# Performance work log

Hardware: AMD Instinct MI355X
Metric: run time of the kernel (lower is better)

## Reference

```python
import jax, jax.numpy as jnp
import numpy as np


def setup_inputs() -> dict:
    key = jax.random.key(0)
    k1, k2, k3, k4 = jax.random.split(key, 4)
    b, h, t, dim, topk = 16, 8, 196, 512, 49
    x = jax.random.normal(k1, (b, t, dim), dtype=jnp.float32)
    adj = jax.random.normal(k2, (b, h, t, t), dtype=jnp.float32)  # per-head routing logits
    Wqkv = jax.random.normal(k3, (dim, 3 * dim), dtype=jnp.float32) * 0.02
    Wv = jax.random.normal(k4, (dim, dim), dtype=jnp.float32) * 0.02
    return {"x": x, "adj": adj, "Wqkv": Wqkv, "Wv": Wv, "topk": topk}


def reference(x, adj, Wqkv, Wv, topk):
    b, t, dim = x.shape
    h = adj.shape[1]
    d = dim // h
    scale = dim ** (-0.5)  # note: full dim, matching source (self.scale = dim**-0.5)

    # qkv projection (stand-in for GIN conv_proj_qkv with nhid = 3*dim)
    qkv = (x @ Wqkv).reshape(b, t, h, 3 * d).transpose(0, 2, 1, 3)  # b h t 3d
    q, k, v = jnp.split(qkv, 3, axis=-1)  # each b h t d

    # TopkRouting: indices of top-k routing logits per (b, h, query-token)
    _, r_idx = jax.lax.top_k(adj, topk)  # b h t topk (r_weight unused: mul_weight='none')

    # KGather: irregular gather of concatenated k/v rows per query token
    kv = jnp.concatenate([k, v], axis=-1).reshape(b * h, t, 2 * d)
    idx = r_idx.reshape(b * h, t, topk)
    kv_sel = jax.vmap(lambda m, i: m[i])(kv, idx)          # (bh, t, topk, 2d)
    kv_sel = kv_sel.reshape(b, h, t, topk, 2 * d)
    k_sel, v_sel = jnp.split(kv_sel, 2, axis=-1)            # b h t topk d

    # small-window attention: each query attends to its topk gathered rows (w^2 = 1)
    attn = jax.nn.softmax(jnp.einsum('bhtd,bhtkd->bhtk', q * scale, k_sel), axis=-1)
    o = jnp.einsum('bhtk,bhtkd->bhtd', attn, v_sel)

    o = o.transpose(0, 2, 1, 3).reshape(b, t, dim)
    o = jax.nn.gelu(o, approximate=False)  # torch F.gelu default = exact erf
    return o @ Wv
```

## Files before the change

### kernel.cpp

```cpp
#include <hip/hip_runtime.h>
#include <hip/hip_bf16.h>
#include <cmath>

#define B_   16
#define H_   8
#define T_   196
#define DIM_ 512
#define DHEAD_ 64
#define TOPK_ 49
#define BT_  (B_ * T_)
#define BH_  (B_ * H_)

#define QB_OFF   0u
#define KB_OFF   1605632u
#define VT_OFF   3211264u
#define XB_OFF   5046272u
#define WQKVT_OFF 6651904u
#define WVT_OFF  7438336u
#define MASK_OFF 7700480u

typedef __bf16 bf16x8 __attribute__((ext_vector_type(8)));
typedef float f32x4 __attribute__((ext_vector_type(4)));

__device__ __forceinline__ unsigned short f2bf(float f) {
    union { float f; unsigned int u; } v; v.f = f;
    const unsigned int u = v.u;
    return (unsigned short)((u + 0x7FFFu + ((u >> 16) & 1u)) >> 16);
}

__device__ __forceinline__ unsigned int ordered_u32(float f) {
    int i = __float_as_int(f);
    return (i < 0) ? ~(unsigned int)i : ((unsigned int)i | 0x80000000u);
}

__device__ __forceinline__ void gload16(const void* g, void* l) {
    __builtin_amdgcn_global_load_lds(
        (const __attribute__((address_space(1))) unsigned int*)g,
        (__attribute__((address_space(3))) unsigned int*)l, 16, 0, 0);
}

__device__ __forceinline__ void route_topk_q(const float* __restrict__ adj,
                                             unsigned int* __restrict__ masks,
                                             const int q, const int lane) {
    const float* arow = adj + (size_t)q * T_;
    const bool v3 = (lane < 4);
    unsigned int u[4];
    u[0] = ordered_u32(arow[lane]);
    u[1] = ordered_u32(arow[lane + 64]);
    u[2] = ordered_u32(arow[lane + 128]);
    u[3] = v3 ? ordered_u32(arow[lane + 192]) : 0u;

    unsigned int w0 = u[0], w1 = u[1], w2 = u[2], w3 = u[3];
    unsigned int prefix = 0u, thr = 0u;
    int k = TOPK_, A = T_;
    for (int b = 31; b >= 0; --b) {
        int C1 = 0;
        C1 += __popcll(__ballot((w0 >> b) == 1u));
        C1 += __popcll(__ballot((w1 >> b) == 1u));
        C1 += __popcll(__ballot((w2 >> b) == 1u));
        C1 += __popcll(__ballot((w3 >> b) == 1u));
        if (C1 >= k) {
            const unsigned int bit = 1u << b;
            prefix |= bit;
            w0 ^= bit; w1 ^= bit; w2 ^= bit; w3 ^= bit;
            A = C1;
        } else { k -= C1; A -= C1; }

        if (k == A || k == 1) {
            const bool mx = (k == 1);
            unsigned int best = mx ? 0u : 0xFFFFFFFFu;
            const unsigned int ww[4] = {w0, w1, w2, w3};
#pragma unroll
            for (int s2 = 0; s2 < 4; ++s2) {
                const bool valid = (s2 < 3) || v3;
                const bool act = valid && ((ww[s2] >> b) == 0u);
                if (act) best = mx ? (u[s2] > best ? u[s2] : best)
                                   : (u[s2] < best ? u[s2] : best);
            }
#pragma unroll
            for (int off = 32; off >= 1; off >>= 1) {
                const unsigned int o = __shfl_xor(best, off);
                best = mx ? (o > best ? o : best) : (o < best ? o : best);
            }
            thr = best;
            break;
        }
        if (b == 0) thr = prefix;
    }

    const unsigned long long lmask = (1ull << lane) - 1ull;
    unsigned long long gm[4];
    int G = 0;
#pragma unroll
    for (int s2 = 0; s2 < 4; ++s2) {
        const bool valid = (s2 < 3) || v3;
        gm[s2] = __ballot(valid && (u[s2] > thr));
        G += __popcll(gm[s2]);
    }
    const int need = TOPK_ - G;
    int cum = 0;
    unsigned long long sb0 = 0, sb1 = 0, sb2 = 0, sb3 = 0;
#pragma unroll
    for (int s2 = 0; s2 < 4; ++s2) {
        const bool valid = (s2 < 3) || v3;
        const bool e = valid && (u[s2] == thr);
        const unsigned long long em = __ballot(e);
        const int rk = cum + __popcll(em & lmask);
        cum += __popcll(em);
        const unsigned long long sel = gm[s2] | __ballot(e && (rk < need));
        if (s2 == 0) sb0 = sel; else if (s2 == 1) sb1 = sel;
        else if (s2 == 2) sb2 = sel; else sb3 = sel;
    }
    if (lane < 8) {
        const unsigned long long mv = (lane < 2) ? sb0 : (lane < 4) ? sb1
                                    : (lane < 6) ? sb2 : sb3;
        const unsigned int wd = (lane & 1) ? (unsigned int)(mv >> 32) : (unsigned int)mv;
        masks[(size_t)q * 8 + lane] = wd;
    }
}

__global__ __launch_bounds__(256) void prep(const float* __restrict__ x,
                                            const float* __restrict__ Wqkv,
                                            unsigned short* __restrict__ xb,
                                            unsigned short* __restrict__ wqkvT) {
    __shared__ unsigned short Tt[64][72];
    const int t = threadIdx.x;
    const int bid = blockIdx.x;

    if (bid < 784) {
        const size_t base = ((size_t)bid * 256 + t) * 8;
        const float4 v0 = *(const float4*)&x[base];
        const float4 v1 = *(const float4*)&x[base + 4];
        uint4 pk;
        pk.x = (unsigned int)f2bf(v0.x) | ((unsigned int)f2bf(v0.y) << 16);
        pk.y = (unsigned int)f2bf(v0.z) | ((unsigned int)f2bf(v0.w) << 16);
        pk.z = (unsigned int)f2bf(v1.x) | ((unsigned int)f2bf(v1.y) << 16);
        pk.w = (unsigned int)f2bf(v1.z) | ((unsigned int)f2bf(v1.w) << 16);
        *(uint4*)&xb[base] = pk;
        return;
    }

    const int b = bid - 784;
    const int tx = b % 24, ty = b / 24;
    const int c0 = tx * 64, r0 = ty * 64;
#pragma unroll
    for (int p = 0; p < 4; ++p) {
        const int r = (t >> 4) + 16 * p;
        const int cl = (t & 15) * 4;
        const float4 v = *(const float4*)&Wqkv[(size_t)(r0 + r) * 1536 + c0 + cl];
        Tt[cl + 0][r] = f2bf(v.x);
        Tt[cl + 1][r] = f2bf(v.y);
        Tt[cl + 2][r] = f2bf(v.z);
        Tt[cl + 3][r] = f2bf(v.w);
    }
    __syncthreads();
#pragma unroll
    for (int p = 0; p < 2; ++p) {
        const int cc = (t >> 3) + 32 * p;
        const int ch = (t & 7) * 8;
        *(uint4*)&wqkvT[(size_t)(c0 + cc) * 512 + r0 + ch] = *(const uint4*)&Tt[cc][ch];
    }
}

template <int BN, int MODE, int FUSE, typename CT>
__global__ __launch_bounds__(256) void gemm_mfma(const unsigned short* __restrict__ A,
                                                 const unsigned short* __restrict__ Bt,
                                                 CT* __restrict__ C,
                                                 const int M, const int N, const int K,
                                                 const float* __restrict__ adj,
                                                 unsigned int* __restrict__ masks,
                                                 unsigned short* __restrict__ vT,
                                                 const float* __restrict__ Wv,
                                                 unsigned short* __restrict__ wvT) {
    constexpr int FN = BN / 32;
    constexpr int CSZ = (MODE == 1) ? 64 * 132 : 1;
    struct ABt { unsigned short A[64][32]; unsigned short B[BN][32]; };
    __shared__ union {
        ABt ab[2];
        unsigned short Cs[CSZ];
        unsigned short Tt[FUSE ? 64 : 1][72];
    } sm;

    const int tid = threadIdx.x;
    const int lane = tid & 63, wid = tid >> 6;
    const int mt = M >> 6;
    const int nGemm = mt * (N / BN);
    const int bid = blockIdx.x;

    if constexpr (FUSE) {
        if (bid >= nGemm) {
            const int rid = bid - nGemm;
            if (rid < 6272) {
                route_topk_q(adj, masks, rid * 4 + wid, lane);
            } else if (rid < 6300) {
                const int e0 = (rid - 6272) * 8192 + tid;
#pragma unroll
                for (int i = 0; i < 32; ++i) {
                    const int e = e0 + i * 256;
                    const int bh = e / 1792;
                    const int rem = e - bh * 1792;
                    const int d = rem / 28;
                    const int tt = rem - d * 28;
                    vT[(size_t)bh * (64 * 224) + (size_t)d * 224 + 196 + tt] = 0;
                }
            } else {
                const int b = rid - 6300;
                const int tx = b & 7, ty = b >> 3;
                const int c0 = tx * 64, r0 = ty * 64;
#pragma unroll
                for (int p = 0; p < 4; ++p) {
                    const int r = (tid >> 4) + 16 * p;
                    const int cl = (tid & 15) * 4;
                    const float4 v = *(const float4*)&Wv[(size_t)(r0 + r) * 512 + c0 + cl];
                    sm.Tt[cl + 0][r] = f2bf(v.x);
                    sm.Tt[cl + 1][r] = f2bf(v.y);
                    sm.Tt[cl + 2][r] = f2bf(v.z);
                    sm.Tt[cl + 3][r] = f2bf(v.w);
                }
                __syncthreads();
#pragma unroll
                for (int p = 0; p < 2; ++p) {
                    const int cc = (tid >> 3) + 32 * p;
                    const int ch = (tid & 7) * 8;
                    *(uint4*)&wvT[(size_t)(c0 + cc) * 512 + r0 + ch] =
                        *(const uint4*)&sm.Tt[cc][ch];
                }
            }
            return;
        }
    }

    const int bx = bid % mt;
    const int by = bid / mt;
    const int row0 = bx * 64;
    const int col0 = by * BN;
    const int wr = wid >> 1, wc = wid & 1;

    f32x4 acc[2][FN];
#pragma unroll
    for (int m = 0; m < 2; ++m)
#pragma unroll
        for (int n = 0; n < FN; ++n)
            acc[m][n] = (f32x4){0.0f, 0.0f, 0.0f, 0.0f};

    const int srow = lane >> 2;
    const int scol = (lane & 3) * 8;
    const unsigned short* aSrc = A + (size_t)(row0 + wid * 16 + srow) * K + scol;
    const unsigned short* bSrc = Bt + (size_t)(col0 + wid * 16 + srow) * K + scol;
    const unsigned short* bSrc2 = bSrc + (size_t)64 * K;

    const int fr = lane & 15;
    const int fk8 = (lane >> 4) * 8;

#define STAGE(BUF) do {                                                        \
        gload16(aSrc, &sm.ab[BUF].A[wid * 16][0]);                             \
        gload16(bSrc, &sm.ab[BUF].B[wid * 16][0]);                             \
        if constexpr (BN == 128) gload16(bSrc2, &sm.ab[BUF].B[64 + wid * 16][0]); \
        aSrc += 32; bSrc += 32; bSrc2 += 32;                                   \
    } while (0)

#define COMPUTE(BUF) do {                                                      \
        bf16x8 af[2], bfv[FN];                                                 \
        _Pragma("unroll")                                                      \
        for (int m = 0; m < 2; ++m)                                            \
            af[m] = *(const bf16x8*)&sm.ab[BUF].A[wr * 32 + m * 16 + fr][fk8]; \
        _Pragma("unroll")                                                      \
        for (int n = 0; n < FN; ++n)                                           \
            bfv[n] = *(const bf16x8*)&sm.ab[BUF].B[wc * (BN / 2) + n * 16 + fr][fk8]; \
        _Pragma("unroll")                                                      \
        for (int m = 0; m < 2; ++m)                                            \
            _Pragma("unroll")                                                  \
            for (int n = 0; n < FN; ++n)                                       \
                acc[m][n] = __builtin_amdgcn_mfma_f32_16x16x32_bf16(af[m], bfv[n], acc[m][n], 0, 0, 0); \
    } while (0)

    STAGE(0);
    __syncthreads();

    for (int k0 = 0; k0 < K; k0 += 64) {
        if (k0 + 32 < K) STAGE(1);
        COMPUTE(0);
        __syncthreads();
        if (k0 + 64 < K) STAGE(0);
        COMPUTE(1);
        __syncthreads();
    }
#undef STAGE
#undef COMPUTE

    if constexpr (MODE == 0) {
#pragma unroll
        for (int m = 0; m < 2; ++m)
#pragma unroll
            for (int n = 0; n < FN; ++n)
#pragma unroll
                for (int i = 0; i < 4; ++i) {
                    const int row = row0 + wr * 32 + m * 16 + (lane >> 4) * 4 + i;
                    const int col = col0 + wc * (BN / 2) + n * 16 + (lane & 15);
                    C[(size_t)row * N + col] = (CT)acc[m][n][i];
                }
    } else {
#pragma unroll
        for (int m = 0; m < 2; ++m)
#pragma unroll
            for (int n = 0; n < FN; ++n)
#pragma unroll
                for (int i = 0; i < 4; ++i) {
                    const int rl = wr * 32 + m * 16 + (lane >> 4) * 4 + i;
                    const int cl = wc * (BN / 2) + n * 16 + (lane & 15);
                    sm.Cs[rl * 132 + cl] = f2bf(acc[m][n][i]);
                }
        __syncthreads();

        unsigned short* ubase = (unsigned short*)C;
#pragma unroll
        for (int ch = 0; ch < BN / 64; ++ch) {
            const int abscol = col0 + ch * 64;
            const int which = (abscol >> 6) % 3;
            const int hh = abscol / 192;
            if (which < 2) {
                const int r = tid >> 2;
                const int co = (tid & 3) * 16;
                const int gr = row0 + r;
                const int bb = gr / T_;
                const int tt = gr - bb * T_;
                const uint2 a0 = *(const uint2*)&sm.Cs[r * 132 + ch * 64 + co];
                const uint2 a1 = *(const uint2*)&sm.Cs[r * 132 + ch * 64 + co + 4];
                const uint2 a2 = *(const uint2*)&sm.Cs[r * 132 + ch * 64 + co + 8];
                const uint2 a3 = *(const uint2*)&sm.Cs[r * 132 + ch * 64 + co + 12];
                unsigned short* dst = ubase + (size_t)which * KB_OFF +
                                      ((size_t)(bb * H_ + hh) * T_ + tt) * DHEAD_ + co;
                uint4 w0; w0.x = a0.x; w0.y = a0.y; w0.z = a1.x; w0.w = a1.y;
                uint4 w1; w1.x = a2.x; w1.y = a2.y; w1.z = a3.x; w1.w = a3.y;
                *(uint4*)&dst[0] = w0;
                *(uint4*)&dst[8] = w1;
            } else {
                const int d = tid >> 2;
                const int j0 = (tid & 3) * 16;
                union { unsigned short s[16]; uint2 v2[4]; } tmp;
#pragma unroll
                for (int j = 0; j < 16; ++j)
                    tmp.s[j] = sm.Cs[(j0 + j) * 132 + ch * 64 + d];
                const int gr0 = row0 + j0;
                const int bb0 = gr0 / T_;
                const int bb1 = (gr0 + 15) / T_;
                if (bb0 == bb1) {
                    const int tt = gr0 - bb0 * T_;
                    unsigned short* dst = ubase + VT_OFF +
                                          (size_t)(bb0 * H_ + hh) * (64 * 224) +
                                          (size_t)d * 224 + tt;
                    *(uint2*)&dst[0]  = tmp.v2[0];
                    *(uint2*)&dst[4]  = tmp.v2[1];
                    *(uint2*)&dst[8]  = tmp.v2[2];
                    *(uint2*)&dst[12] = tmp.v2[3];
                } else {
#pragma unroll
                    for (int j = 0; j < 16; ++j) {
                        const int gr = gr0 + j;
                        const int bb = gr / T_;
                        const int tt = gr - bb * T_;
                        ubase[VT_OFF + (size_t)(bb * H_ + hh) * (64 * 224) +
                              (size_t)d * 224 + tt] = tmp.s[j];
                    }
                }
            }
        }
    }
}

__global__ __launch_bounds__(64) void attn_mfma(const unsigned short* __restrict__ qb,
                                                const unsigned short* __restrict__ kb,
                                                const unsigned short* __restrict__ vT,
                                                const unsigned int* __restrict__ masks,
                                                unsigned short* __restrict__ obuf) {
    __shared__ unsigned int mask_lds[16][8];
    __shared__ unsigned short P[16][232];

    const int lane = threadIdx.x;
    const int qt = blockIdx.x;
    const int bh = blockIdx.y;
    const int bb = bh >> 3, hh = bh & 7;
    const int q0 = qt * 16;

#pragma unroll
    for (int s2 = 0; s2 < 2; ++s2) {
        const int e = lane + s2 * 64;
        const int r = e >> 3, wd = e & 7;
        const int t = q0 + r;
        mask_lds[r][wd] = (t < T_) ? masks[((size_t)bh * T_ + t) * 8 + wd] : 0u;
    }
    *(unsigned long long*)&P[lane >> 2][208 + (lane & 3) * 4] = 0ull;
    __syncthreads();

    const int fr = lane & 15;
    const int fk8 = (lane >> 4) * 8;
    const unsigned short* qbh = qb + ((size_t)bh * T_ + q0) * DHEAD_;
    const unsigned short* kbh = kb + (size_t)bh * T_ * DHEAD_;

    const bf16x8 aq0 = *(const bf16x8*)&qbh[fr * 64 + fk8];
    const bf16x8 aq1 = *(const bf16x8*)&qbh[fr * 64 + 32 + fk8];

    f32x4 s[13];
#pragma unroll
    for (int c = 0; c < 13; ++c) s[c] = (f32x4){0.0f, 0.0f, 0.0f, 0.0f};
    __builtin_amdgcn_s_setprio(1);
#pragma unroll
    for (int c = 0; c < 13; ++c) {
        const bf16x8 b0 = *(const bf16x8*)&kbh[(c * 16 + fr) * 64 + fk8];
        const bf16x8 b1 = *(const bf16x8*)&kbh[(c * 16 + fr) * 64 + 32 + fk8];
        s[c] = __builtin_amdgcn_mfma_f32_16x16x32_bf16(aq0, b0, s[c], 0, 0, 0);
        s[c] = __builtin_amdgcn_mfma_f32_16x16x32_bf16(aq1, b1, s[c], 0, 0, 0);
    }
    __builtin_amdgcn_s_setprio(0);

    const float scale = 0.044194173824159216f;
    float l0 = 0, l1 = 0, l2 = 0, l3 = 0;
#pragma unroll
    for (int i = 0; i < 4; ++i) {
        const int rowl = (lane >> 4) * 4 + i;
        float li = 0.0f;
#pragma unroll
        for (int c = 0; c < 13; ++c) {
            const unsigned int mw = mask_lds[rowl][c >> 1];
            const bool sel = (mw >> (((c & 1) << 4) + fr)) & 1u;
            const float pv = sel ? __expf(s[c][i] * scale) : 0.0f;
            P[rowl][c * 16 + fr] = f2bf(pv);
            li += pv;
        }
        if (i == 0) l0 = li; else if (i == 1) l1 = li;
        else if (i == 2) l2 = li; else l3 = li;
    }
#pragma unroll
    for (int off = 8; off >= 1; off >>= 1) {
        l0 += __shfl_xor(l0, off);
        l1 += __shfl_xor(l1, off);
        l2 += __shfl_xor(l2, off);
        l3 += __shfl_xor(l3, off);
    }
    const float rl0 = 1.0f / l0, rl1 = 1.0f / l1, rl2 = 1.0f / l2, rl3 = 1.0f / l3;

    const unsigned short* vbh = vT + (size_t)bh * (64 * 224);
    f32x4 o[4];
#pragma unroll
    for (int n = 0; n < 4; ++n) o[n] = (f32x4){0.0f, 0.0f, 0.0f, 0.0f};
    __builtin_amdgcn_s_setprio(1);
#pragma unroll
    for (int kk = 0; kk < 7; ++kk) {
        const bf16x8 ap = *(const bf16x8*)&P[fr][kk * 32 + fk8];
#pragma unroll
        for (int n = 0; n < 4; ++n) {
            const bf16x8 bv = *(const bf16x8*)&vbh[(n * 16 + fr) * 224 + kk * 32 + fk8];
            o[n] = __builtin_amdgcn_mfma_f32_16x16x32_bf16(ap, bv, o[n], 0, 0, 0);
        }
    }
    __builtin_amdgcn_s_setprio(0);

#pragma unroll
    for (int i = 0; i < 4; ++i) {
        const float rl = (i == 0) ? rl0 : (i == 1) ? rl1 : (i == 2) ? rl2 : rl3;
        const int t = q0 + (lane >> 4) * 4 + i;
        if (t < T_) {
            unsigned short* orow = obuf + ((size_t)(bb * T_ + t)) * DIM_ + hh * DHEAD_;
#pragma unroll
            for (int n = 0; n < 4; ++n) {
                const float ov = o[n][i] * rl;
                const float g = 0.5f * ov * (1.0f + erff(ov * 0.70710678118654752f));
                orow[n * 16 + fr] = f2bf(g);
            }
        }
    }
}

extern "C" void kernel_launch(void* const* d_in, const int* in_sizes, int n_in,
                              void* d_out, int out_size, void* d_ws, size_t ws_size,
                              hipStream_t stream) {
    const float* x    = (const float*)d_in[0];
    const float* adj  = (const float*)d_in[1];
    const float* Wqkv = (const float*)d_in[2];
    const float* Wv   = (const float*)d_in[3];
    float* out = (float*)d_out;
    unsigned short* ub = (unsigned short*)d_ws;

    unsigned short* qb    = ub + QB_OFF;
    unsigned short* kb    = ub + KB_OFF;
    unsigned short* vT    = ub + VT_OFF;
    unsigned short* xb    = ub + XB_OFF;
    unsigned short* wqkvT = ub + WQKVT_OFF;
    unsigned short* wvT   = ub + WVT_OFF;
    unsigned int*   masks = (unsigned int*)(ub + MASK_OFF);

    prep<<<976, 256, 0, stream>>>(x, Wqkv, xb, wqkvT);

    gemm_mfma<128, 1, 1, unsigned short><<<6952, 256, 0, stream>>>(
        xb, wqkvT, ub, BT_, 3 * DIM_, DIM_, adj, masks, vT, Wv, wvT);

    attn_mfma<<<dim3(13, BH_), 64, 0, stream>>>(qb, kb, vT, masks, xb);

    gemm_mfma<64, 0, 0, float><<<392, 256, 0, stream>>>(
        xb, wvT, out, BT_, DIM_, DIM_, nullptr, nullptr, nullptr, nullptr, nullptr);
}
```

Baseline: 64.20 us.

## Rebalance top-k routing across prep and QKV GEMM; widen attention query tiles

Half of the top-k routing work, plus the Wv transpose and the vT pad zeroing, moves from the QKV GEMM launch into the prep kernel. This balances the two launches so the routing overlaps with the conversion work. Each attention block now handles 32 queries instead of 16, so every K and V fragment load feeds two MFMA tiles. That roughly halves the number of blocks and raises register and LDS use per block, which can reduce parallelism over the 128 heads.

```diff
diff --git a/kernel.cpp b/kernel.cpp
--- a/kernel.cpp
+++ b/kernel.cpp
@@ -18,6 +18,8 @@
 #define WQKVT_OFF 6651904u
 #define WVT_OFF  7438336u
 #define MASK_OFF 7700480u
+
+#define QSPLIT_BLOCKS 3136
 
 typedef __bf16 bf16x8 __attribute__((ext_vector_type(8)));
 typedef float f32x4 __attribute__((ext_vector_type(4)));
@@ -121,14 +123,24 @@
 
 __global__ __launch_bounds__(256) void prep(const float* __restrict__ x,
                                             const float* __restrict__ Wqkv,
+                                            const float* __restrict__ Wv,
+                                            const float* __restrict__ adj,
                                             unsigned short* __restrict__ xb,
-                                            unsigned short* __restrict__ wqkvT) {
+                                            unsigned short* __restrict__ wqkvT,
+                                            unsigned short* __restrict__ wvT,
+                                            unsigned short* __restrict__ vT,
+                                            unsigned int* __restrict__ masks) {
     __shared__ unsigned short Tt[64][72];
     const int t = threadIdx.x;
     const int bid = blockIdx.x;
 
-    if (bid < 784) {
-        const size_t base = ((size_t)bid * 256 + t) * 8;
+    if (bid < QSPLIT_BLOCKS) {
+        route_topk_q(adj, masks, bid * 4 + (t >> 6), t & 63);
+        return;
+    }
+    int b2 = bid - QSPLIT_BLOCKS;
+    if (b2 < 784) {
+        const size_t base = ((size_t)b2 * 256 + t) * 8;
         const float4 v0 = *(const float4*)&x[base];
         const float4 v1 = *(const float4*)&x[base + 4];
         uint4 pk;
@@ -139,15 +151,32 @@
         *(uint4*)&xb[base] = pk;
         return;
     }
-
-    const int b = bid - 784;
-    const int tx = b % 24, ty = b / 24;
+    b2 -= 784;
+    if (b2 >= 192 && b2 < 220) {
+        const int e0 = (b2 - 192) * 8192 + t;
+#pragma unroll
+        for (int i = 0; i < 32; ++i) {
+            const int e = e0 + i * 256;
+            const int bh = e / 1792;
+            const int rem = e - bh * 1792;
+            const int d = rem / 28;
+            const int tt = rem - d * 28;
+            vT[(size_t)bh * (64 * 224) + (size_t)d * 224 + 196 + tt] = 0;
+        }
+        return;
+    }
+
+    const float* src;
+    unsigned short* dst;
+    int Cc, tx, ty;
+    if (b2 < 192) { src = Wqkv; dst = wqkvT; Cc = 1536; tx = b2 % 24; ty = b2 / 24; }
+    else { const int b = b2 - 220; src = Wv; dst = wvT; Cc = 512; tx = b & 7; ty = b >> 3; }
     const int c0 = tx * 64, r0 = ty * 64;
 #pragma unroll
     for (int p = 0; p < 4; ++p) {
         const int r = (t >> 4) + 16 * p;
         const int cl = (t & 15) * 4;
-        const float4 v = *(const float4*)&Wqkv[(size_t)(r0 + r) * 1536 + c0 + cl];
+        const float4 v = *(const float4*)&src[(size_t)(r0 + r) * Cc + c0 + cl];
         Tt[cl + 0][r] = f2bf(v.x);
         Tt[cl + 1][r] = f2bf(v.y);
         Tt[cl + 2][r] = f2bf(v.z);
@@ -158,7 +187,7 @@
     for (int p = 0; p < 2; ++p) {
         const int cc = (t >> 3) + 32 * p;
         const int ch = (t & 7) * 8;
-        *(uint4*)&wqkvT[(size_t)(c0 + cc) * 512 + r0 + ch] = *(const uint4*)&Tt[cc][ch];
+        *(uint4*)&dst[(size_t)(c0 + cc) * 512 + r0 + ch] = *(const uint4*)&Tt[cc][ch];
     }
 }
 
@@ -168,17 +197,13 @@
                                                  CT* __restrict__ C,
                                                  const int M, const int N, const int K,
                                                  const float* __restrict__ adj,
-                                                 unsigned int* __restrict__ masks,
-                                                 unsigned short* __restrict__ vT,
-                                                 const float* __restrict__ Wv,
-                                                 unsigned short* __restrict__ wvT) {
+                                                 unsigned int* __restrict__ masks) {
     constexpr int FN = BN / 32;
     constexpr int CSZ = (MODE == 1) ? 64 * 132 : 1;
     struct ABt { unsigned short A[64][32]; unsigned short B[BN][32]; };
     __shared__ union {
         ABt ab[2];
         unsigned short Cs[CSZ];
-        unsigned short Tt[FUSE ? 64 : 1][72];
     } sm;
 
     const int tid = threadIdx.x;
@@ -190,42 +215,7 @@
     if constexpr (FUSE) {
         if (bid >= nGemm) {
             const int rid = bid - nGemm;
-            if (rid < 6272) {
-                route_topk_q(adj, masks, rid * 4 + wid, lane);
-            } else if (rid < 6300) {
-                const int e0 = (rid - 6272) * 8192 + tid;
-#pragma unroll
-                for (int i = 0; i < 32; ++i) {
-                    const int e = e0 + i * 256;
-                    const int bh = e / 1792;
-                    const int rem = e - bh * 1792;
-                    const int d = rem / 28;
-                    const int tt = rem - d * 28;
-                    vT[(size_t)bh * (64 * 224) + (size_t)d * 224 + 196 + tt] = 0;
-                }
-            } else {
-                const int b = rid - 6300;
-                const int tx = b & 7, ty = b >> 3;
-                const int c0 = tx * 64, r0 = ty * 64;
-#pragma unroll
-                for (int p = 0; p < 4; ++p) {
-                    const int r = (tid >> 4) + 16 * p;
-                    const int cl = (tid & 15) * 4;
-                    const float4 v = *(const float4*)&Wv[(size_t)(r0 + r) * 512 + c0 + cl];
-                    sm.Tt[cl + 0][r] = f2bf(v.x);
-                    sm.Tt[cl + 1][r] = f2bf(v.y);
-                    sm.Tt[cl + 2][r] = f2bf(v.z);
-                    sm.Tt[cl + 3][r] = f2bf(v.w);
-                }
-                __syncthreads();
-#pragma unroll
-                for (int p = 0; p < 2; ++p) {
-                    const int cc = (tid >> 3) + 32 * p;
-                    const int ch = (tid & 7) * 8;
-                    *(uint4*)&wvT[(size_t)(c0 + cc) * 512 + r0 + ch] =
-                        *(const uint4*)&sm.Tt[cc][ch];
-                }
-            }
+            route_topk_q(adj, masks, QSPLIT_BLOCKS * 4 + rid * 4 + wid, lane);
             return;
         }
     }
@@ -373,23 +363,30 @@
                                                 const unsigned short* __restrict__ vT,
                                                 const unsigned int* __restrict__ masks,
                                                 unsigned short* __restrict__ obuf) {
-    __shared__ unsigned int mask_lds[16][8];
-    __shared__ unsigned short P[16][232];
+    __shared__ unsigned int mask_lds[32][8];
+    __shared__ unsigned short P[32][232];
 
     const int lane = threadIdx.x;
     const int qt = blockIdx.x;
     const int bh = blockIdx.y;
     const int bb = bh >> 3, hh = bh & 7;
-    const int q0 = qt * 16;
-
-#pragma unroll
-    for (int s2 = 0; s2 < 2; ++s2) {
-        const int e = lane + s2 * 64;
+    const int q0 = qt * 32;
+
+#pragma unroll
+    for (int p = 0; p < 4; ++p) {
+        const int e = lane + p * 64;
         const int r = e >> 3, wd = e & 7;
         const int t = q0 + r;
         mask_lds[r][wd] = (t < T_) ? masks[((size_t)bh * T_ + t) * 8 + wd] : 0u;
     }
-    *(unsigned long long*)&P[lane >> 2][208 + (lane & 3) * 4] = 0ull;
+#pragma unroll
+    for (int p = 0; p < 2; ++p) {
+        const int e = lane + p * 64;
+        if (e < 96) {
+            const int r = e & 31, c8 = e >> 5;
+            *(uint4*)&P[r][208 + c8 * 8] = (uint4){0u, 0u, 0u, 0u};
+        }
+    }
     __syncthreads();
 
     const int fr = lane & 15;
@@ -397,78 +394,94 @@
     const unsigned short* qbh = qb + ((size_t)bh * T_ + q0) * DHEAD_;
     const unsigned short* kbh = kb + (size_t)bh * T_ * DHEAD_;
 
-    const bf16x8 aq0 = *(const bf16x8*)&qbh[fr * 64 + fk8];
-    const bf16x8 aq1 = *(const bf16x8*)&qbh[fr * 64 + 32 + fk8];
-
-    f32x4 s[13];
-#pragma unroll
-    for (int c = 0; c < 13; ++c) s[c] = (f32x4){0.0f, 0.0f, 0.0f, 0.0f};
+    const bf16x8 aq00 = *(const bf16x8*)&qbh[fr * 64 + fk8];
+    const bf16x8 aq01 = *(const bf16x8*)&qbh[fr * 64 + 32 + fk8];
+    const bf16x8 aq10 = *(const bf16x8*)&qbh[(16 + fr) * 64 + fk8];
+    const bf16x8 aq11 = *(const bf16x8*)&qbh[(16 + fr) * 64 + 32 + fk8];
+
+    f32x4 s0[13], s1[13];
+#pragma unroll
+    for (int c = 0; c < 13; ++c) {
+        s0[c] = (f32x4){0.0f, 0.0f, 0.0f, 0.0f};
+        s1[c] = (f32x4){0.0f, 0.0f, 0.0f, 0.0f};
+    }
     __builtin_amdgcn_s_setprio(1);
 #pragma unroll
     for (int c = 0; c < 13; ++c) {
         const bf16x8 b0 = *(const bf16x8*)&kbh[(c * 16 + fr) * 64 + fk8];
         const bf16x8 b1 = *(const bf16x8*)&kbh[(c * 16 + fr) * 64 + 32 + fk8];
-        s[c] = __builtin_amdgcn_mfma_f32_16x16x32_bf16(aq0, b0, s[c], 0, 0, 0);
-        s[c] = __builtin_amdgcn_mfma_f32_16x16x32_bf16(aq1, b1, s[c], 0, 0, 0);
+        s0[c] = __builtin_amdgcn_mfma_f32_16x16x32_bf16(aq00, b0, s0[c], 0, 0, 0);
+        s0[c] = __builtin_amdgcn_mfma_f32_16x16x32_bf16(aq01, b1, s0[c], 0, 0, 0);
+        s1[c] = __builtin_amdgcn_mfma_f32_16x16x32_bf16(aq10, b0, s1[c], 0, 0, 0);
+        s1[c] = __builtin_amdgcn_mfma_f32_16x16x32_bf16(aq11, b1, s1[c], 0, 0, 0);
     }
     __builtin_amdgcn_s_setprio(0);
 
     const float scale = 0.044194173824159216f;
-    float l0 = 0, l1 = 0, l2 = 0, l3 = 0;
-#pragma unroll
-    for (int i = 0; i < 4; ++i) {
-        const int rowl = (lane >> 4) * 4 + i;
-        float li = 0.0f;
-#pragma unroll
-        for (int c = 0; c < 13; ++c) {
-            const unsigned int mw = mask_lds[rowl][c >> 1];
-            const bool sel = (mw >> (((c & 1) << 4) + fr)) & 1u;
-            const float pv = sel ? __expf(s[c][i] * scale) : 0.0f;
-            P[rowl][c * 16 + fr] = f2bf(pv);
-            li += pv;
-        }
-        if (i == 0) l0 = li; else if (i == 1) l1 = li;
-        else if (i == 2) l2 = li; else l3 = li;
-    }
-#pragma unroll
-    for (int off = 8; off >= 1; off >>= 1) {
-        l0 += __shfl_xor(l0, off);
-        l1 += __shfl_xor(l1, off);
-        l2 += __shfl_xor(l2, off);
-        l3 += __shfl_xor(l3, off);
-    }
-    const float rl0 = 1.0f / l0, rl1 = 1.0f / l1, rl2 = 1.0f / l2, rl3 = 1.0f / l3;
+    float lv[8];
+#pragma unroll
+    for (int tau = 0; tau < 2; ++tau)
+#pragma unroll
+        for (int i = 0; i < 4; ++i) {
+            const int rowl = tau * 16 + (lane >> 4) * 4 + i;
+            float li = 0.0f;
+#pragma unroll
+            for (int c = 0; c < 13; ++c) {
+                const unsigned int mw = mask_lds[rowl][c >> 1];
+                const bool sel = (mw >> (((c & 1) << 4) + fr)) & 1u;
+                const float sv = (tau == 0) ? s0[c][i] : s1[c][i];
+                const float pv = sel ? __expf(sv * scale) : 0.0f;
+                P[rowl][c * 16 + fr] = f2bf(pv);
+                li += pv;
+            }
+            lv[tau * 4 + i] = li;
+        }
+#pragma unroll
+    for (int off = 8; off >= 1; off >>= 1)
+#pragma unroll
+        for (int j = 0; j < 8; ++j)
+            lv[j] += __shfl_xor(lv[j], off);
+    float rl[8];
+#pragma unroll
+    for (int j = 0; j < 8; ++j) rl[j] = 1.0f / lv[j];
 
     const unsigned short* vbh = vT + (size_t)bh * (64 * 224);
-    f32x4 o[4];
-#pragma unroll
-    for (int n = 0; n < 4; ++n) o[n] = (f32x4){0.0f, 0.0f, 0.0f, 0.0f};
+    f32x4 o0[4], o1[4];
+#pragma unroll
+    for (int n = 0; n < 4; ++n) {
+        o0[n] = (f32x4){0.0f, 0.0f, 0.0f, 0.0f};
+        o1[n] = (f32x4){0.0f, 0.0f, 0.0f, 0.0f};
+    }
     __builtin_amdgcn_s_setprio(1);
 #pragma unroll
     for (int kk = 0; kk < 7; ++kk) {
-        const bf16x8 ap = *(const bf16x8*)&P[fr][kk * 32 + fk8];
+        const bf16x8 ap0 = *(const bf16x8*)&P[fr][kk * 32 + fk8];
+        const bf16x8 ap1 = *(const bf16x8*)&P[16 + fr][kk * 32 + fk8];
 #pragma unroll
         for (int n = 0; n < 4; ++n) {
             const bf16x8 bv = *(const bf16x8*)&vbh[(n * 16 + fr) * 224 + kk * 32 + fk8];
-            o[n] = __builtin_amdgcn_mfma_f32_16x16x32_bf16(ap, bv, o[n], 0, 0, 0);
+            o0[n] = __builtin_amdgcn_mfma_f32_16x16x32_bf16(ap0, bv, o0[n], 0, 0, 0);
+            o1[n] = __builtin_amdgcn_mfma_f32_16x16x32_bf16(ap1, bv, o1[n], 0, 0, 0);
         }
     }
     __builtin_amdgcn_s_setprio(0);
 
 #pragma unroll
-    for (int i = 0; i < 4; ++i) {
-        const float rl = (i == 0) ? rl0 : (i == 1) ? rl1 : (i == 2) ? rl2 : rl3;
-        const int t = q0 + (lane >> 4) * 4 + i;
-        if (t < T_) {
-            unsigned short* orow = obuf + ((size_t)(bb * T_ + t)) * DIM_ + hh * DHEAD_;
-#pragma unroll
-            for (int n = 0; n < 4; ++n) {
-                const float ov = o[n][i] * rl;
-                const float g = 0.5f * ov * (1.0f + erff(ov * 0.70710678118654752f));
-                orow[n * 16 + fr] = f2bf(g);
+    for (int tau = 0; tau < 2; ++tau)
+#pragma unroll
+        for (int i = 0; i < 4; ++i) {
+            const float rli = rl[tau * 4 + i];
+            const int t = q0 + tau * 16 + (lane >> 4) * 4 + i;
+            if (t < T_) {
+                unsigned short* orow = obuf + ((size_t)(bb * T_ + t)) * DIM_ + hh * DHEAD_;
+#pragma unroll
+                for (int n = 0; n < 4; ++n) {
+                    const float ov = ((tau == 0) ? o0[n][i] : o1[n][i]) * rli;
+                    const float g = 0.5f * ov * (1.0f + erff(ov * 0.70710678118654752f));
+                    orow[n * 16 + fr] = f2bf(g);
+                }
             }
         }
-    }
 }
 
 extern "C" void kernel_launch(void* const* d_in, const int* in_sizes, int n_in,
@@ -489,13 +502,13 @@
     unsigned short* wvT   = ub + WVT_OFF;
     unsigned int*   masks = (unsigned int*)(ub + MASK_OFF);
 
-    prep<<<976, 256, 0, stream>>>(x, Wqkv, xb, wqkvT);
-
-    gemm_mfma<128, 1, 1, unsigned short><<<6952, 256, 0, stream>>>(
-        xb, wqkvT, ub, BT_, 3 * DIM_, DIM_, adj, masks, vT, Wv, wvT);
-
-    attn_mfma<<<dim3(13, BH_), 64, 0, stream>>>(qb, kb, vT, masks, xb);
+    prep<<<4204, 256, 0, stream>>>(x, Wqkv, Wv, adj, xb, wqkvT, wvT, vT, masks);
+
+    gemm_mfma<128, 1, 1, unsigned short><<<3724, 256, 0, stream>>>(
+        xb, wqkvT, ub, BT_, 3 * DIM_, DIM_, adj, masks);
+
+    attn_mfma<<<dim3(7, BH_), 64, 0, stream>>>(qb, kb, vT, masks, xb);
 
     gemm_mfma<64, 0, 0, float><<<392, 256, 0, stream>>>(
-        xb, wvT, out, BT_, DIM_, DIM_, nullptr, nullptr, nullptr, nullptr, nullptr);
-}
+        xb, wvT, out, BT_, DIM_, DIM_, nullptr, nullptr);
+}
```

New measurement: 67.54 us. 5.2% more time.
